# Kernel optimization log

Hardware: AMD Instinct MI355X
Metric: run time of the kernel (lower is better)

Reference implementation:

```python
import jax, jax.numpy as jnp
import numpy as np

EPS = 1e-12  # matches torch F.normalize eps


def _l2_normalize(v, axis):
    n = jnp.sqrt(jnp.sum(v * v, axis=axis, keepdims=True))
    return v / jnp.maximum(n, EPS)


def setup_inputs() -> dict:
    key = jax.random.key(0)
    k1, k2 = jax.random.split(key)
    N, D, K = 131072, 512, 64
    x = jax.random.normal(k1, (N, D), dtype=jnp.float32)
    clusters = jax.random.normal(k2, (K, D), dtype=jnp.float32)
    alpha = jnp.ones((), dtype=jnp.float32)
    return {"x": x, "clusters": clusters, "alpha": alpha}


def reference(x, clusters, alpha):
    # cosine similarity between normalized features and normalized codebook
    normed_clusters = _l2_normalize(clusters, axis=1)   # [K, D]
    normed_features = _l2_normalize(x, axis=-1)         # [N, D]
    inner_products = jnp.einsum('nd,kd->nk', normed_features, normed_clusters)  # [N, K]
    # alpha is not None branch: soft assignment
    cluster_probs = jax.nn.softmax(inner_products * alpha, axis=1)  # [N, K]
    cluster_loss = -jnp.mean(jnp.sum(cluster_probs * inner_products, axis=1))
    return cluster_loss, cluster_probs
```

## Files before the change

kernel.cpp:

```cpp
#include <hip/hip_runtime.h>
#include <hip/hip_bf16.h>

#define NROWS 131072
#define DIM   512
#define NK    64

typedef __attribute__((ext_vector_type(4))) float f32x4;
typedef __attribute__((ext_vector_type(8))) short s16x8;

static __device__ __forceinline__ unsigned pk2(float a, float b) {
    union { __hip_bfloat162 h; unsigned u; } cv;
    cv.h = __float22bfloat162_rn(make_float2(a, b));
    return cv.u;
}

__global__ void prep_kernel(const float* __restrict__ cl,
                            unsigned* __restrict__ cb,
                            float* __restrict__ loss_out) {
    const int k = blockIdx.x, t = threadIdx.x;
    const float4* rp = reinterpret_cast<const float4*>(cl + k * DIM);
    float4 f0 = rp[2 * t], f1 = rp[2 * t + 1];
    float ss = f0.x*f0.x + f0.y*f0.y + f0.z*f0.z + f0.w*f0.w
             + f1.x*f1.x + f1.y*f1.y + f1.z*f1.z + f1.w*f1.w;
#pragma unroll
    for (int m = 1; m < 64; m <<= 1) ss += __shfl_xor(ss, m, 64);
    const float rn = 1.0f / fmaxf(sqrtf(ss), 1e-12f);
    uint4 o;
    o.x = pk2(f0.x * rn, f0.y * rn);
    o.y = pk2(f0.z * rn, f0.w * rn);
    o.z = pk2(f1.x * rn, f1.y * rn);
    o.w = pk2(f1.z * rn, f1.w * rn);
    reinterpret_cast<uint4*>(cb + (size_t)k * (DIM / 2))[t] = o;
    if (k == 0 && t == 0) *loss_out = 0.0f;
}

__global__ __launch_bounds__(512, 4) void fused_kernel(
        const float* __restrict__ x,
        const unsigned* __restrict__ cb,
        const float* __restrict__ alphap,
        float* __restrict__ out) {
    __shared__ unsigned short ldsb[NK * DIM];

    for (int u = threadIdx.x; u < NK * DIM / 8; u += blockDim.x) {
        const int r = u >> 6, c6 = u & 63;
        const uint4 v = reinterpret_cast<const uint4*>(cb)[u];
        *reinterpret_cast<uint4*>(&ldsb[r * DIM + ((c6 ^ (r & 7)) << 3)]) = v;
    }
    __syncthreads();

    const float alpha = alphap[0];
    const int lane = threadIdx.x & 63;
    const int n = lane & 15;
    const int q = lane >> 4;
    const int sw = n & 7;
    const int gw = (int)((blockIdx.x * blockDim.x + threadIdx.x) >> 6);
    const int nw = (int)((gridDim.x * blockDim.x) >> 6);

    const unsigned short* b_base = &ldsb[n * DIM];
    float* __restrict__ probs = out + 1;

    float lossa = 0.0f;

    for (int g = gw; g < NROWS / 16; g += nw) {
        const int row0 = g << 4;
        const float4* xp4 = reinterpret_cast<const float4*>(
            x + (size_t)(row0 + n) * DIM + (q << 3));
        f32x4 a0 = {0.f,0.f,0.f,0.f}, a1 = {0.f,0.f,0.f,0.f};
        f32x4 a2 = {0.f,0.f,0.f,0.f}, a3 = {0.f,0.f,0.f,0.f};
        float ss = 0.0f;

        float4 c0 = xp4[0], c1 = xp4[1];
        float4 d0 = xp4[8], d1 = xp4[9];
#pragma unroll
        for (int t = 0; t < 16; t++) {
            float4 e0v, e1v;
            if (t < 14) { e0v = xp4[(t + 2) * 8]; e1v = xp4[(t + 2) * 8 + 1]; }
            ss += c0.x*c0.x + c0.y*c0.y + c0.z*c0.z + c0.w*c0.w
                + c1.x*c1.x + c1.y*c1.y + c1.z*c1.z + c1.w*c1.w;
            union { s16x8 v; unsigned u[4]; } A;
            A.u[0] = pk2(c0.x, c0.y); A.u[1] = pk2(c0.z, c0.w);
            A.u[2] = pk2(c1.x, c1.y); A.u[3] = pk2(c1.z, c1.w);
            const int off = (((t << 2) | q) ^ sw) << 3;
            const s16x8 b0 = *reinterpret_cast<const s16x8*>(b_base + off);
            const s16x8 b1 = *reinterpret_cast<const s16x8*>(b_base + 16 * DIM + off);
            const s16x8 b2 = *reinterpret_cast<const s16x8*>(b_base + 32 * DIM + off);
            const s16x8 b3 = *reinterpret_cast<const s16x8*>(b_base + 48 * DIM + off);
            a0 = __builtin_amdgcn_mfma_f32_16x16x32_bf16(A.v, b0, a0, 0, 0, 0);
            a1 = __builtin_amdgcn_mfma_f32_16x16x32_bf16(A.v, b1, a1, 0, 0, 0);
            a2 = __builtin_amdgcn_mfma_f32_16x16x32_bf16(A.v, b2, a2, 0, 0, 0);
            a3 = __builtin_amdgcn_mfma_f32_16x16x32_bf16(A.v, b3, a3, 0, 0, 0);
            c0 = d0; c1 = d1; d0 = e0v; d1 = e1v;
        }

        ss += __shfl_xor(ss, 16, 64);
        ss += __shfl_xor(ss, 32, 64);
        const float rnorm = 1.0f / fmaxf(sqrtf(ss), 1e-12f);

#pragma unroll
        for (int r = 0; r < 4; r++) {
            const float rn = __shfl(rnorm, (q << 2) + r, 64);
            const float i0 = a0[r] * rn, i1 = a1[r] * rn, i2 = a2[r] * rn, i3 = a3[r] * rn;
            const float z0 = i0 * alpha, z1 = i1 * alpha, z2 = i2 * alpha, z3 = i3 * alpha;
            float mx = fmaxf(fmaxf(z0, z1), fmaxf(z2, z3));
#pragma unroll
            for (int m = 1; m < 16; m <<= 1) mx = fmaxf(mx, __shfl_xor(mx, m, 64));
            const float e0 = __expf(z0 - mx), e1 = __expf(z1 - mx);
            const float e2 = __expf(z2 - mx), e3 = __expf(z3 - mx);
            float s  = e0 + e1 + e2 + e3;
            float sl = e0 * i0 + e1 * i1 + e2 * i2 + e3 * i3;
#pragma unroll
            for (int m = 1; m < 16; m <<= 1) {
                s  += __shfl_xor(s,  m, 64);
                sl += __shfl_xor(sl, m, 64);
            }
            const float inv = 1.0f / s;
            float* __restrict__ pr = probs + (size_t)(row0 + (q << 2) + r) * NK + n;
            pr[0]  = e0 * inv;
            pr[16] = e1 * inv;
            pr[32] = e2 * inv;
            pr[48] = e3 * inv;
            if (n == 0) lossa += sl * inv;
        }
    }

    lossa += __shfl_xor(lossa, 16, 64);
    lossa += __shfl_xor(lossa, 32, 64);
    if (lane == 0) atomicAdd(out, -lossa * (1.0f / NROWS));
}

extern "C" void kernel_launch(void* const* d_in, const int* in_sizes, int n_in,
                              void* d_out, int out_size, void* d_ws, size_t ws_size,
                              hipStream_t stream) {
    const float* x  = (const float*)d_in[0];
    const float* cl = (const float*)d_in[1];
    const float* al = (const float*)d_in[2];
    float* out = (float*)d_out;
    unsigned* cb = (unsigned*)d_ws;

    prep_kernel<<<dim3(NK), dim3(64), 0, stream>>>(cl, cb, out);
    fused_kernel<<<dim3(512), dim3(512), 0, stream>>>(x, cb, al, out);
}
```

Before: 500.5 us.

## Deepen x prefetch and coalesce probability stores via lane shuffles

Raises the register prefetch depth for x rows from two to four k-steps, keeping more global loads in flight. It also replaces the scattered per-lane probability stores with a shuffle-based transpose, so each wave writes a whole contiguous 64-float output row per step. The output is offset by one float (the loss slot), which the shuffle pattern handles by shifting lanes. This costs extra shuffles and register pressure and relies on fragile index arithmetic.

```diff
diff --git a/kernel.cpp b/kernel.cpp
--- a/kernel.cpp
+++ b/kernel.cpp
@@ -57,7 +57,6 @@
     const int nw = (int)((gridDim.x * blockDim.x) >> 6);
 
     const unsigned short* b_base = &ldsb[n * DIM];
-    float* __restrict__ probs = out + 1;
 
     float lossa = 0.0f;
 
@@ -69,12 +68,13 @@
         f32x4 a2 = {0.f,0.f,0.f,0.f}, a3 = {0.f,0.f,0.f,0.f};
         float ss = 0.0f;
 
-        float4 c0 = xp4[0], c1 = xp4[1];
-        float4 d0 = xp4[8], d1 = xp4[9];
+        float4 pf0[4], pf1[4];
+#pragma unroll
+        for (int j = 0; j < 4; j++) { pf0[j] = xp4[j * 8]; pf1[j] = xp4[j * 8 + 1]; }
 #pragma unroll
         for (int t = 0; t < 16; t++) {
-            float4 e0v, e1v;
-            if (t < 14) { e0v = xp4[(t + 2) * 8]; e1v = xp4[(t + 2) * 8 + 1]; }
+            const float4 c0 = pf0[t & 3], c1 = pf1[t & 3];
+            if (t < 12) { pf0[t & 3] = xp4[(t + 4) * 8]; pf1[t & 3] = xp4[(t + 4) * 8 + 1]; }
             ss += c0.x*c0.x + c0.y*c0.y + c0.z*c0.z + c0.w*c0.w
                 + c1.x*c1.x + c1.y*c1.y + c1.z*c1.z + c1.w*c1.w;
             union { s16x8 v; unsigned u[4]; } A;
@@ -89,13 +89,13 @@
             a1 = __builtin_amdgcn_mfma_f32_16x16x32_bf16(A.v, b1, a1, 0, 0, 0);
             a2 = __builtin_amdgcn_mfma_f32_16x16x32_bf16(A.v, b2, a2, 0, 0, 0);
             a3 = __builtin_amdgcn_mfma_f32_16x16x32_bf16(A.v, b3, a3, 0, 0, 0);
-            c0 = d0; c1 = d1; d0 = e0v; d1 = e1v;
         }
 
         ss += __shfl_xor(ss, 16, 64);
         ss += __shfl_xor(ss, 32, 64);
         const float rnorm = 1.0f / fmaxf(sqrtf(ss), 1e-12f);
 
+        float p[4][4];
 #pragma unroll
         for (int r = 0; r < 4; r++) {
             const float rn = __shfl(rnorm, (q << 2) + r, 64);
@@ -114,13 +114,32 @@
                 sl += __shfl_xor(sl, m, 64);
             }
             const float inv = 1.0f / s;
-            float* __restrict__ pr = probs + (size_t)(row0 + (q << 2) + r) * NK + n;
-            pr[0]  = e0 * inv;
-            pr[16] = e1 * inv;
-            pr[32] = e2 * inv;
-            pr[48] = e3 * inv;
+            p[r][0] = e0 * inv;
+            p[r][1] = e1 * inv;
+            p[r][2] = e2 * inv;
+            p[r][3] = e3 * inv;
             if (n == 0) lossa += sl * inv;
         }
+
+#pragma unroll
+        for (int k = 0; k < 16; k++) {
+            const int rs = k & 3;
+            const int src = ((k >> 2) << 4) | ((lane - 1) & 15);
+            const float t0 = __shfl(p[rs][0], src, 64);
+            const float t1 = __shfl(p[rs][1], src, 64);
+            const float t2 = __shfl(p[rs][2], src, 64);
+            const float t3 = __shfl(p[rs][3], src, 64);
+            const int rp = (k == 0) ? 0 : ((k - 1) & 3);
+            const int qp = (k == 0) ? 0 : ((k - 1) >> 2);
+            const float tp = __shfl(p[rp][3], (qp << 4) | 15, 64);
+            const int cs = ((lane - 1) >> 4) & 3;
+            float v = cs == 0 ? t0 : (cs == 1 ? t1 : (cs == 2 ? t2 : t3));
+            if (lane == 0) v = tp;
+            if (k > 0 || lane > 0)
+                out[(size_t)(row0 + k) * 64 + lane] = v;
+        }
+        if (lane == 63)
+            out[(size_t)(row0 + 16) * 64] = p[3][3];
     }
 
     lossa += __shfl_xor(lossa, 16, 64);
```

New measurement: 591.6 us. 1.18x slower.

## Split K dimension across waves with register-resident codebook and LDS reduction

Applied to the files above, without the earlier changes.

Each of the 8 waves in a block now owns a 64-wide slice of the feature dimension and keeps its matching codebook fragments in registers, which removes the full LDS codebook copy and its per-step LDS reads. Partial dot products and squared norms are reduced across waves through LDS, and each wave then does a full-row softmax over 64 lanes. Probabilities are staged in LDS so each row is written as a contiguous 64-float store, with a one-element offset for the loss slot. The cost is three block barriers per 16-row group, a fixed grid of 512 blocks each handling 16 groups with double-buffered loads, and a launch bound lowered to 2 blocks per SIMD.

```diff
diff --git a/kernel.cpp b/kernel.cpp
--- a/kernel.cpp
+++ b/kernel.cpp
@@ -4,6 +4,7 @@
 #define NROWS 131072
 #define DIM   512
 #define NK    64
+#define GPB   16
 
 typedef __attribute__((ext_vector_type(4))) float f32x4;
 typedef __attribute__((ext_vector_type(8))) short s16x8;
@@ -12,6 +13,12 @@
     union { __hip_bfloat162 h; unsigned u; } cv;
     cv.h = __float22bfloat162_rn(make_float2(a, b));
     return cv.u;
+}
+
+static __device__ __forceinline__ void lds_barrier() {
+    asm volatile("s_waitcnt lgkmcnt(0)" ::: "memory");
+    __builtin_amdgcn_s_barrier();
+    asm volatile("" ::: "memory");
 }
 
 __global__ void prep_kernel(const float* __restrict__ cl,
@@ -34,97 +41,125 @@
     if (k == 0 && t == 0) *loss_out = 0.0f;
 }
 
-__global__ __launch_bounds__(512, 4) void fused_kernel(
+__global__ __launch_bounds__(512, 2) void fused_kernel(
         const float* __restrict__ x,
         const unsigned* __restrict__ cb,
         const float* __restrict__ alphap,
         float* __restrict__ out) {
-    __shared__ unsigned short ldsb[NK * DIM];
+    __shared__ float part[8][16][65];
+    __shared__ float ssp[8][16];
 
-    for (int u = threadIdx.x; u < NK * DIM / 8; u += blockDim.x) {
-        const int r = u >> 6, c6 = u & 63;
-        const uint4 v = reinterpret_cast<const uint4*>(cb)[u];
-        *reinterpret_cast<uint4*>(&ldsb[r * DIM + ((c6 ^ (r & 7)) << 3)]) = v;
-    }
-    __syncthreads();
+    const int tid  = threadIdx.x;
+    const int lane = tid & 63, wid = tid >> 6;
+    const int n = lane & 15, q = lane >> 4;
+
+    const s16x8* cbv = reinterpret_cast<const s16x8*>(cb);
+    const int tb = (wid << 3) + q;
+    const s16x8 bf00 = cbv[(n)      * 64 + tb],     bf01 = cbv[(n)      * 64 + tb + 4];
+    const s16x8 bf10 = cbv[(n + 16) * 64 + tb],     bf11 = cbv[(n + 16) * 64 + tb + 4];
+    const s16x8 bf20 = cbv[(n + 32) * 64 + tb],     bf21 = cbv[(n + 32) * 64 + tb + 4];
+    const s16x8 bf30 = cbv[(n + 48) * 64 + tb],     bf31 = cbv[(n + 48) * 64 + tb + 4];
 
     const float alpha = alphap[0];
-    const int lane = threadIdx.x & 63;
-    const int n = lane & 15;
-    const int q = lane >> 4;
-    const int sw = n & 7;
-    const int gw = (int)((blockIdx.x * blockDim.x + threadIdx.x) >> 6);
-    const int nw = (int)((gridDim.x * blockDim.x) >> 6);
-
-    const unsigned short* b_base = &ldsb[n * DIM];
-    float* __restrict__ probs = out + 1;
+    const int g0 = (int)blockIdx.x * GPB;
+    const size_t lrow = (size_t)n * DIM + (wid << 6) + (q << 3);
 
     float lossa = 0.0f;
 
-    for (int g = gw; g < NROWS / 16; g += nw) {
-        const int row0 = g << 4;
-        const float4* xp4 = reinterpret_cast<const float4*>(
-            x + (size_t)(row0 + n) * DIM + (q << 3));
-        f32x4 a0 = {0.f,0.f,0.f,0.f}, a1 = {0.f,0.f,0.f,0.f};
-        f32x4 a2 = {0.f,0.f,0.f,0.f}, a3 = {0.f,0.f,0.f,0.f};
-        float ss = 0.0f;
-
-        float4 c0 = xp4[0], c1 = xp4[1];
-        float4 d0 = xp4[8], d1 = xp4[9];
-#pragma unroll
-        for (int t = 0; t < 16; t++) {
-            float4 e0v, e1v;
-            if (t < 14) { e0v = xp4[(t + 2) * 8]; e1v = xp4[(t + 2) * 8 + 1]; }
-            ss += c0.x*c0.x + c0.y*c0.y + c0.z*c0.z + c0.w*c0.w
-                + c1.x*c1.x + c1.y*c1.y + c1.z*c1.z + c1.w*c1.w;
-            union { s16x8 v; unsigned u[4]; } A;
-            A.u[0] = pk2(c0.x, c0.y); A.u[1] = pk2(c0.z, c0.w);
-            A.u[2] = pk2(c1.x, c1.y); A.u[3] = pk2(c1.z, c1.w);
-            const int off = (((t << 2) | q) ^ sw) << 3;
-            const s16x8 b0 = *reinterpret_cast<const s16x8*>(b_base + off);
-            const s16x8 b1 = *reinterpret_cast<const s16x8*>(b_base + 16 * DIM + off);
-            const s16x8 b2 = *reinterpret_cast<const s16x8*>(b_base + 32 * DIM + off);
-            const s16x8 b3 = *reinterpret_cast<const s16x8*>(b_base + 48 * DIM + off);
-            a0 = __builtin_amdgcn_mfma_f32_16x16x32_bf16(A.v, b0, a0, 0, 0, 0);
-            a1 = __builtin_amdgcn_mfma_f32_16x16x32_bf16(A.v, b1, a1, 0, 0, 0);
-            a2 = __builtin_amdgcn_mfma_f32_16x16x32_bf16(A.v, b2, a2, 0, 0, 0);
-            a3 = __builtin_amdgcn_mfma_f32_16x16x32_bf16(A.v, b3, a3, 0, 0, 0);
-            c0 = d0; c1 = d1; d0 = e0v; d1 = e1v;
-        }
-
+    auto process = [&](int gi, const float4& c0, const float4& c1,
+                       const float4& d0, const float4& d1) {
+        const int row0 = (g0 + gi) << 4;
+        float ss = c0.x*c0.x + c0.y*c0.y + c0.z*c0.z + c0.w*c0.w
+                 + c1.x*c1.x + c1.y*c1.y + c1.z*c1.z + c1.w*c1.w
+                 + d0.x*d0.x + d0.y*d0.y + d0.z*d0.z + d0.w*d0.w
+                 + d1.x*d1.x + d1.y*d1.y + d1.z*d1.z + d1.w*d1.w;
         ss += __shfl_xor(ss, 16, 64);
         ss += __shfl_xor(ss, 32, 64);
-        const float rnorm = 1.0f / fmaxf(sqrtf(ss), 1e-12f);
+        if (lane < 16) ssp[wid][lane] = ss;
+
+        f32x4 a0 = {0.f,0.f,0.f,0.f}, a1 = a0, a2 = a0, a3 = a0;
+        union { s16x8 v; unsigned u[4]; } A;
+        A.u[0] = pk2(c0.x, c0.y); A.u[1] = pk2(c0.z, c0.w);
+        A.u[2] = pk2(c1.x, c1.y); A.u[3] = pk2(c1.z, c1.w);
+        a0 = __builtin_amdgcn_mfma_f32_16x16x32_bf16(A.v, bf00, a0, 0, 0, 0);
+        a1 = __builtin_amdgcn_mfma_f32_16x16x32_bf16(A.v, bf10, a1, 0, 0, 0);
+        a2 = __builtin_amdgcn_mfma_f32_16x16x32_bf16(A.v, bf20, a2, 0, 0, 0);
+        a3 = __builtin_amdgcn_mfma_f32_16x16x32_bf16(A.v, bf30, a3, 0, 0, 0);
+        A.u[0] = pk2(d0.x, d0.y); A.u[1] = pk2(d0.z, d0.w);
+        A.u[2] = pk2(d1.x, d1.y); A.u[3] = pk2(d1.z, d1.w);
+        a0 = __builtin_amdgcn_mfma_f32_16x16x32_bf16(A.v, bf01, a0, 0, 0, 0);
+        a1 = __builtin_amdgcn_mfma_f32_16x16x32_bf16(A.v, bf11, a1, 0, 0, 0);
+        a2 = __builtin_amdgcn_mfma_f32_16x16x32_bf16(A.v, bf21, a2, 0, 0, 0);
+        a3 = __builtin_amdgcn_mfma_f32_16x16x32_bf16(A.v, bf31, a3, 0, 0, 0);
 
 #pragma unroll
-        for (int r = 0; r < 4; r++) {
-            const float rn = __shfl(rnorm, (q << 2) + r, 64);
-            const float i0 = a0[r] * rn, i1 = a1[r] * rn, i2 = a2[r] * rn, i3 = a3[r] * rn;
-            const float z0 = i0 * alpha, z1 = i1 * alpha, z2 = i2 * alpha, z3 = i3 * alpha;
-            float mx = fmaxf(fmaxf(z0, z1), fmaxf(z2, z3));
+        for (int rr = 0; rr < 4; rr++) {
+            const int cr = (q << 2) + rr;
+            part[wid][cr][n]      = a0[rr];
+            part[wid][cr][n + 16] = a1[rr];
+            part[wid][cr][n + 32] = a2[rr];
+            part[wid][cr][n + 48] = a3[rr];
+        }
+        lds_barrier();
+
 #pragma unroll
-            for (int m = 1; m < 16; m <<= 1) mx = fmaxf(mx, __shfl_xor(mx, m, 64));
-            const float e0 = __expf(z0 - mx), e1 = __expf(z1 - mx);
-            const float e2 = __expf(z2 - mx), e3 = __expf(z3 - mx);
-            float s  = e0 + e1 + e2 + e3;
-            float sl = e0 * i0 + e1 * i1 + e2 * i2 + e3 * i3;
+        for (int e = 0; e < 2; e++) {
+            const int k = (wid << 1) + e;
+            const float sv = ssp[0][k] + ssp[1][k] + ssp[2][k] + ssp[3][k]
+                           + ssp[4][k] + ssp[5][k] + ssp[6][k] + ssp[7][k];
+            const float c  = part[0][k][lane] + part[1][k][lane] + part[2][k][lane]
+                           + part[3][k][lane] + part[4][k][lane] + part[5][k][lane]
+                           + part[6][k][lane] + part[7][k][lane];
+            const float rn = 1.0f / fmaxf(sqrtf(sv), 1e-12f);
+            const float ip = c * rn;
+            const float z  = ip * alpha;
+            float mx = z;
 #pragma unroll
-            for (int m = 1; m < 16; m <<= 1) {
+            for (int m = 1; m < 64; m <<= 1) mx = fmaxf(mx, __shfl_xor(mx, m, 64));
+            const float ev = __expf(z - mx);
+            float s = ev, sl = ev * ip;
+#pragma unroll
+            for (int m = 1; m < 64; m <<= 1) {
                 s  += __shfl_xor(s,  m, 64);
                 sl += __shfl_xor(sl, m, 64);
             }
             const float inv = 1.0f / s;
-            float* __restrict__ pr = probs + (size_t)(row0 + (q << 2) + r) * NK + n;
-            pr[0]  = e0 * inv;
-            pr[16] = e1 * inv;
-            pr[32] = e2 * inv;
-            pr[48] = e3 * inv;
-            if (n == 0) lossa += sl * inv;
+            part[0][k][lane] = ev * inv;
+            if (lane == 0) lossa += sl * inv;
         }
+        lds_barrier();
+
+        const float* cf = &part[0][0][0];
+#pragma unroll
+        for (int e = 0; e < 2; e++) {
+            const int k = (wid << 1) + e;
+            if (k > 0 || lane > 0) {
+                const int ei = (k << 6) + lane - 1;
+                out[(size_t)(row0 + k) * 64 + lane] = cf[(ei >> 6) * 65 + (ei & 63)];
+            }
+        }
+        if (tid == 0) out[(size_t)(row0 + 16) * 64] = cf[15 * 65 + 63];
+        lds_barrier();
+    };
+
+    float4 Aa, Ab, Ac, Ad, Ba, Bb, Bc, Bd;
+    {
+        const float4* p = reinterpret_cast<const float4*>(x + (size_t)(g0 << 4) * DIM + lrow);
+        Aa = p[0]; Ab = p[1]; Ac = p[8]; Ad = p[9];
+    }
+    for (int gi = 0; gi < GPB; gi += 2) {
+        {   const float4* p = reinterpret_cast<const float4*>(
+                x + (size_t)((g0 + gi + 1) << 4) * DIM + lrow);
+            Ba = p[0]; Bb = p[1]; Bc = p[8]; Bd = p[9]; }
+        process(gi, Aa, Ab, Ac, Ad);
+        if (gi + 2 < GPB) {
+            const float4* p = reinterpret_cast<const float4*>(
+                x + (size_t)((g0 + gi + 2) << 4) * DIM + lrow);
+            Aa = p[0]; Ab = p[1]; Ac = p[8]; Ad = p[9];
+        }
+        process(gi + 1, Ba, Bb, Bc, Bd);
     }
 
-    lossa += __shfl_xor(lossa, 16, 64);
-    lossa += __shfl_xor(lossa, 32, 64);
     if (lane == 0) atomicAdd(out, -lossa * (1.0f / NROWS));
 }
 
@@ -138,5 +173,5 @@
     unsigned* cb = (unsigned*)d_ws;
 
     prep_kernel<<<dim3(NK), dim3(64), 0, stream>>>(cl, cb, out);
-    fused_kernel<<<dim3(512), dim3(512), 0, stream>>>(x, cb, al, out);
+    fused_kernel<<<dim3(NROWS / 16 / GPB), dim3(512), 0, stream>>>(x, cb, al, out);
 }
```

New measurement: 406.8 us. -18.7%, faster.
